# Kernel tuning notes

Hardware: AMD Instinct MI355X
Metric: run time of the kernel (lower is better)

The kernel has to match this reference:

```python
import jax, jax.numpy as jnp
import numpy as np

R = 3
D = 2 * R + 1            # 7 displacements per axis
B, C, H, W = 2, 128, 48, 96
EPS = 1e-5


def conv2d(x, w, stride=1, padding=1):
    return jax.lax.conv_general_dilated(
        x, w, (stride, stride), [(padding, padding), (padding, padding)],
        dimension_numbers=('NCHW', 'OIHW', 'NCHW'))


def deconv2d(x, w, stride=2, padding=1):
    # w: torch ConvTranspose2d layout (I, O, kh, kw)
    wf = jnp.flip(w, (2, 3)).transpose(1, 0, 2, 3)  # -> OIHW, spatially flipped
    p = w.shape[2] - 1 - padding
    return jax.lax.conv_general_dilated(
        x, wf, (1, 1), [(p, p), (p, p)], lhs_dilation=(stride, stride),
        dimension_numbers=('NCHW', 'OIHW', 'NCHW'))


def bn_relu(x, g, b):
    # BatchNorm2d, training-mode statistics (biased variance), then ReLU
    mu = x.mean(axis=(0, 2, 3), keepdims=True)
    var = x.var(axis=(0, 2, 3), keepdims=True)
    xn = (x - mu) * jax.lax.rsqrt(var + EPS)
    return jax.nn.relu(xn * g[None, :, None, None] + b[None, :, None, None])


def grid_sample_zeros(img, gx, gy):
    # img: (B,C,H,W); gx, gy: (B,S) pixel coords. Bilinear, zero padding,
    # align_corners=True (coords already in pixel space -> identity unnormalize).
    b, c, h, w = img.shape
    x0 = jnp.floor(gx)
    y0 = jnp.floor(gy)
    wx = gx - x0
    wy = gy - y0
    imgf = img.reshape(b, c, h * w)

    def corner(xi, yi, wgt):
        valid = (xi >= 0) & (xi < w) & (yi >= 0) & (yi < h)
        xi_c = jnp.clip(xi, 0, w - 1).astype(jnp.int32)
        yi_c = jnp.clip(yi, 0, h - 1).astype(jnp.int32)
        lin = (yi_c * w + xi_c)[:, None, :]            # (B,1,S)
        v = jnp.take_along_axis(imgf, lin, axis=2)     # (B,C,S)
        return v * (wgt * valid)[:, None, :]

    return (corner(x0, y0, (1 - wx) * (1 - wy))
            + corner(x0 + 1, y0, wx * (1 - wy))
            + corner(x0, y0 + 1, (1 - wx) * wy)
            + corner(x0 + 1, y0 + 1, wx * wy))


def setup_inputs() -> dict:
    key = jax.random.key(0)
    ks = jax.random.split(key, 24)
    s = 0.05
    f1 = jax.random.normal(ks[0], (B, C, H, W), dtype=jnp.float32)
    f2 = jax.random.normal(ks[1], (B, C, H, W), dtype=jnp.float32)
    cx = jax.random.uniform(ks[2], (B, 1, H, W), dtype=jnp.float32) * (W - 1)
    cy = jax.random.uniform(ks[3], (B, 1, H, W), dtype=jnp.float32) * (H - 1)
    coords = jnp.concatenate([cx, cy], axis=1)  # (B,2,H,W): [x, y]
    p = {
        'w1': jax.random.normal(ks[4], (96, 2 * C, 3, 3)) * s,
        'g1': jnp.ones((96,)), 'b1': jnp.zeros((96,)),
        'w2': jax.random.normal(ks[5], (128, 96, 3, 3)) * s,
        'g2': jnp.ones((128,)), 'b2': jnp.zeros((128,)),
        'w3': jax.random.normal(ks[6], (128, 128, 3, 3)) * s,
        'g3': jnp.ones((128,)), 'b3': jnp.zeros((128,)),
        'w4': jax.random.normal(ks[7], (64, 128, 3, 3)) * s,
        'g4': jnp.ones((64,)), 'b4': jnp.zeros((64,)),
        'w5': jax.random.normal(ks[8], (64, 32, 4, 4)) * s,  # ConvTranspose (I,O,kh,kw)
        'g5': jnp.ones((32,)), 'b5': jnp.zeros((32,)),
        'w6': jax.random.normal(ks[9], (1, 32, 3, 3)) * s,
        'b6': jnp.zeros((1,)),
        'dap_w': jnp.eye(D * D, dtype=jnp.float32),  # identity init
    }
    return {'f1': f1, 'f2': f2, 'coords': coords, **p}


def reference(f1, f2, coords, w1, g1, b1, w2, g2, b2, w3, g3, b3,
              w4, g4, b4, w5, g5, b5, w6, b6, dap_w):
    b, c, h, w = f1.shape
    dx = jnp.linspace(-R, R, D)
    delta = jnp.stack(jnp.meshgrid(dx, dx, indexing='ij'), axis=-1)  # (D,D,2)
    cen = (coords.transpose(0, 2, 3, 1).reshape(b, 1, h, 1, w, 2)
           + delta.reshape(1, D, 1, D, 1, 2))                        # (B,D,H,D,W,2)
    gx = cen[..., 0].reshape(b, -1)
    gy = cen[..., 1].reshape(b, -1)
    f2s = grid_sample_zeros(f2, gx, gy).reshape(b, c, D, h, D, w)
    f2s = f2s.transpose(0, 2, 4, 1, 3, 5)                            # (B,D,D,C,H,W)
    f1e = jnp.broadcast_to(f1[:, None, None], (b, D, D, c, h, w))
    corr = jnp.concatenate([f1e, f2s], axis=3).reshape(b * D * D, 2 * c, h, w)
    x = bn_relu(conv2d(corr, w1), g1, b1)
    x = bn_relu(conv2d(x, w2, stride=2), g2, b2)
    x = bn_relu(conv2d(x, w3), g3, b3)
    x = bn_relu(conv2d(x, w4), g4, b4)
    x = bn_relu(deconv2d(x, w5), g5, b5)
    x = conv2d(x, w6) + b6[None, :, None, None]
    cost = x.reshape(b, D * D, h, w)
    cost = jnp.einsum('ed,bdhw->behw', dap_w, cost)  # DAP 1x1 conv, no bias
    return cost  # (B, (2r+1)^2, H, W)
```

## Files before the change

kernel.cpp:

```cpp
#include <hip/hip_runtime.h>
#include <hip/hip_bf16.h>

using bf16 = __hip_bfloat16;
typedef __attribute__((ext_vector_type(8))) short s8v;
typedef __attribute__((ext_vector_type(4))) float f4v;
typedef __attribute__((ext_vector_type(16))) float f16v;

static constexpr int Bb = 2, Hh = 48, Ww = 96;
static constexpr int HW = Hh * Ww;
static constexpr int DD = 49, Nn = Bb * DD;
static constexpr int H2 = 24, W2 = 48, HW2 = H2 * W2;

static constexpr size_t off_wf1a = 0;
static constexpr size_t off_wf1b = 221184;
static constexpr size_t off_wf3  = 442368;
static constexpr size_t off_wf2  = 737280;
static constexpr size_t off_wf4  = 958464;
static constexpr size_t off_wf5  = 1105920;
static constexpr size_t off_f1t  = 1171456;
static constexpr size_t off_y1a  = 3530752;
static constexpr size_t off_stats= 7069696;
static constexpr size_t off_f2s  = 7079936;
static constexpr size_t off_y1   = 122685440;
static constexpr size_t off_f2t  = off_y1;
static constexpr size_t off_y2   = off_f2s;
static constexpr size_t off_y3   = off_f2s + 28901376;
static constexpr size_t off_y4   = off_f2s + 57802752;
static constexpr size_t off_y5   = off_f2s + 72253440;
static constexpr size_t off_y6   = off_f2s + 101154816;
static constexpr size_t WS_NEEDED = 209389568;

__device__ __forceinline__ float bf2f(unsigned short h) {
  return __uint_as_float(((unsigned)h) << 16);
}
__device__ __forceinline__ unsigned short f2bf(float f) {
  __hip_bfloat16 h = __float2bfloat16(f);
  union { __hip_bfloat16 x; unsigned short u; } cv; cv.x = h; return cv.u;
}
template<bool EN>
__device__ __forceinline__ uint4 bn8(uint4 v, const float* a, const float* b, int c0) {
  if constexpr (!EN) return v;
  union { uint4 u; unsigned short h[8]; } X; X.u = v;
#pragma unroll
  for (int i = 0; i < 8; ++i) {
    float f = fmaxf(bf2f(X.h[i]) * a[c0 + i] + b[c0 + i], 0.f);
    X.h[i] = f2bf(f);
  }
  return X.u;
}
__device__ __forceinline__ s8v as_s8v(uint4 v) {
  union { uint4 u; s8v s; } cv; cv.u = v; return cv.s;
}
__device__ __forceinline__ int swz(int icl) { return ((icl >> 1) ^ (icl >> 3)) & 3; }

__global__ __launch_bounds__(256) void zero_k(float* __restrict__ p, int n) {
  int i = blockIdx.x * 256 + threadIdx.x;
  if (i < n) p[i] = 0.f;
}

__global__ __launch_bounds__(256) void tr_f2_k(const float* __restrict__ f2, float* __restrict__ f2t) {
  int o = blockIdx.x * 256 + threadIdx.x;
  if (o >= 2 * HW * 16) return;
  int c8 = o & 15; int pos = (o >> 4) % HW; int b = o / (HW * 16);
  float v[8];
#pragma unroll
  for (int i = 0; i < 8; ++i) v[i] = f2[((size_t)(b * 128 + c8 * 8 + i)) * HW + pos];
  float* dst = f2t + ((size_t)b * HW + pos) * 128 + c8 * 8;
#pragma unroll
  for (int i = 0; i < 8; ++i) dst[i] = v[i];
}

__global__ __launch_bounds__(256) void tr_f1_k(const float* __restrict__ f1, bf16* __restrict__ f1t) {
  int o = blockIdx.x * 256 + threadIdx.x;
  if (o >= 2 * HW * 16) return;
  int c8 = o & 15; int pos = (o >> 4) % HW; int b = o / (HW * 16);
  union { uint4 u; unsigned short h[8]; } Y;
#pragma unroll
  for (int i = 0; i < 8; ++i) Y.h[i] = f2bf(f1[((size_t)(b * 128 + c8 * 8 + i)) * HW + pos]);
  *(uint4*)(f1t + ((size_t)b * HW + pos) * 128 + c8 * 8) = Y.u;
}

__global__ __launch_bounds__(256)
void prep32_k(const float* __restrict__ w, uint4* __restrict__ wf, int NT, int CINT, int ciOff) {
  int idx = blockIdx.x * 256 + threadIdx.x;
  int total = 9 * 2 * 4 * NT * 64;
  if (idx >= total) return;
  int ocl = idx & 31; int lh = (idx >> 5) & 1;
  int q = idx >> 6; int nt = q % NT; int rest = q / NT;
  int ks = rest & 3; int cih = (rest >> 2) & 1; int khw = rest >> 3;
  int oc = nt * 32 + ocl;
  union { uint4 u; unsigned short h[8]; } Y;
#pragma unroll
  for (int i = 0; i < 8; ++i) {
    int ci = ciOff + cih * 64 + ks * 16 + lh * 8 + i;
    Y.h[i] = f2bf(w[((size_t)oc * CINT + ci) * 9 + khw]);
  }
  wf[idx] = Y.u;
}

__global__ __launch_bounds__(256)
void prep16_k(const float* __restrict__ w, uint4* __restrict__ wf, int NT, int CINT,
              int NSTAGE, int CPS, int KPS) {
  int idx = blockIdx.x * 256 + threadIdx.x;
  int total = 9 * NSTAGE * KPS * NT * 64;
  if (idx >= total) return;
  int ocl = idx & 15; int lg = (idx >> 4) & 3;
  int q = idx >> 6; int nt = q % NT; int q2 = q / NT;
  int ks = q2 % KPS; int q3 = q2 / KPS;
  int st = q3 % NSTAGE; int khw = q3 / NSTAGE;
  int oc = nt * 16 + ocl;
  union { uint4 u; unsigned short h[8]; } Y;
#pragma unroll
  for (int i = 0; i < 8; ++i) {
    int ci = st * CPS + ks * 32 + lg * 8 + i;
    Y.h[i] = f2bf(w[((size_t)oc * CINT + ci) * 9 + khw]);
  }
  wf[idx] = Y.u;
}

__global__ __launch_bounds__(256)
void prep_w5_k(const float* __restrict__ w5, uint4* __restrict__ wf) {
  int idx = blockIdx.x * 256 + threadIdx.x;
  if (idx >= 4096) return;
  int ocl = idx & 15; int lg = (idx >> 4) & 3;
  int nt = (idx >> 6) & 1; int ks = (idx >> 7) & 7; int p = idx >> 10;
  int ph = p >> 1, pw = p & 1;
  int t = ks >> 2, u = (ks >> 1) & 1;
  int kh = 3 - ph - 2 * t, kw = 3 - pw - 2 * u;
  int oc = nt * 16 + ocl;
  union { uint4 u4; unsigned short h[8]; } Y;
#pragma unroll
  for (int i = 0; i < 8; ++i) {
    int ci = (ks & 1) * 32 + lg * 8 + i;
    Y.h[i] = f2bf(w5[(((size_t)ci * 32 + oc) * 4 + kh) * 4 + kw]);
  }
  wf[idx] = Y.u4;
}

__global__ __launch_bounds__(256)
void sample_k(const float* __restrict__ f2t, const float* __restrict__ coords,
              bf16* __restrict__ f2s) {
  int wv = blockIdx.x * 4 + (threadIdx.x >> 6);
  int lane = threadIdx.x & 63;
  int p0 = wv * 32;
  for (int k = 0; k < 32; ++k) {
    int P = p0 + k;
    int hw = P % HW; int n = P / HW;
    int b = n / DD, d = n % DD;
    float gx = coords[(size_t)b * 2 * HW + hw] + (float)(d / 7 - 3);
    float gy = coords[((size_t)b * 2 + 1) * HW + hw] + (float)(d % 7 - 3);
    float x0f = floorf(gx), y0f = floorf(gy);
    float wx = gx - x0f, wy = gy - y0f;
    int x0 = (int)x0f, y0 = (int)y0f;
    const float* base = f2t + (size_t)b * HW * 128;
    float r0 = 0.f, r1 = 0.f;
#pragma unroll
    for (int c = 0; c < 4; ++c) {
      int xi = x0 + (c & 1), yi = y0 + (c >> 1);
      float wgt = ((c & 1) ? wx : 1.f - wx) * ((c >> 1) ? wy : 1.f - wy);
      if (xi < 0 || xi >= Ww || yi < 0 || yi >= Hh) wgt = 0.f;
      int xc = min(max(xi, 0), Ww - 1), yc = min(max(yi, 0), Hh - 1);
      const float* pv = base + ((size_t)(yc * Ww + xc)) * 128 + 2 * lane;
      r0 += wgt * pv[0];
      r1 += wgt * pv[1];
    }
    unsigned pack = (unsigned)f2bf(r0) | ((unsigned)f2bf(r1) << 16);
    ((unsigned*)f2s)[(size_t)P * 64 + lane] = pack;
  }
}

template<int NLD, int NTHR, int NGRAN, int IC, int CIN>
__device__ __forceinline__ void stage_issue(const bf16* __restrict__ in, size_t inbase,
    int ih0, int iw0, int HI, int WI, int ksl, int tid, uint4 (&stg)[NLD]) {
#pragma unroll
  for (int t = 0; t < NLD; ++t) {
    int idx = tid + t * NTHR;
    uint4 v = make_uint4(0u, 0u, 0u, 0u);
    if (idx < NGRAN) {
      int h8 = idx & 3; int pix = idx >> 2;
      int icl = pix % IC, ihl = pix / IC;
      int ih = ih0 + ihl, iw = iw0 + icl;
      if (ih >= 0 && ih < HI && iw >= 0 && iw < WI)
        v = *(const uint4*)(in + inbase + ((size_t)(ih * WI + iw)) * CIN + ksl * 32 + h8 * 8);
    }
    stg[t] = v;
  }
}

template<int NLD, int NTHR, int NGRAN, int IC, int ROWB, bool HAS_BN>
__device__ __forceinline__ void stage_commit(char* __restrict__ lds,
    const float* __restrict__ a, const float* __restrict__ b,
    int ih0, int iw0, int HI, int WI, int ksl, int tid, uint4 (&stg)[NLD]) {
#pragma unroll
  for (int t = 0; t < NLD; ++t) {
    int idx = tid + t * NTHR;
    if (idx < NGRAN) {
      int h8 = idx & 3; int pix = idx >> 2;
      int icl = pix % IC, ihl = pix / IC;
      uint4 v = stg[t];
      if constexpr (HAS_BN) {
        int ih = ih0 + ihl, iw = iw0 + icl;
        if (ih >= 0 && ih < HI && iw >= 0 && iw < WI) v = bn8<true>(v, a, b, ksl * 32 + h8 * 8);
      }
      int g = h8 ^ swz(icl);
      *(uint4*)(lds + (ihl * IC + icl) * ROWB + g * 16) = v;
    }
  }
}

template<int COUT, int NT, int MT, int NB, int GR, int GC, int CIN,
         bool OUTF32, bool HAS_BASE, bool HAS_BN, bool HAS_STATS>
__global__ __launch_bounds__(((GR * GC) / MT) * (NT / NB) * 64)
void conv32_k(const bf16* __restrict__ in, const uint4* __restrict__ wf,
              void* __restrict__ outv, const float* __restrict__ base,
              const float* __restrict__ bn_a, const float* __restrict__ bn_b,
              float* __restrict__ stats, int N, int H, int W, int DIV) {
  constexpr int NW = ((GR * GC) / MT) * (NT / NB);
  constexpr int NTHR = NW * 64;
  constexpr int BR = GR * 2, BC = GC * 16;
  constexpr int IR = BR + 2, IC = BC + 2;
  constexpr int NSL = CIN / 32;
  constexpr int NGRAN = IR * IC * 4;
  constexpr int NLD = (NGRAN + NTHR - 1) / NTHR;
  __shared__ __align__(16) char lds[IR * IC * 64];

  const int tid = threadIdx.x;
  const int lane = tid & 63;
  const int wv = tid >> 6;
  const int lm = lane & 31, lh = lane >> 5;
  const int dh = lm >> 4, dw = lm & 15;
  constexpr int NG = NT / NB;
  const int mg = wv / NG, ng = wv % NG;

  const int tW = W / BC, tH = H / BR;
  const int tile = blockIdx.x % (tH * tW);
  const int n = blockIdx.x / (tH * tW);
  const int oh0 = (tile / tW) * BR, ow0 = (tile % tW) * BC;
  const int ih0 = oh0 - 1, iw0 = ow0 - 1;
  const size_t inbase = (size_t)n * H * W * CIN;

  int trA[MT], tcA[MT];
#pragma unroll
  for (int i = 0; i < MT; ++i) { int mt = mg * MT + i; trA[i] = mt / GC; tcA[i] = mt % GC; }

  f16v acc[MT][NB];
#pragma unroll
  for (int i = 0; i < MT; ++i)
#pragma unroll
    for (int j = 0; j < NB; ++j)
#pragma unroll
      for (int r = 0; r < 16; ++r) acc[i][j][r] = 0.f;

  {
    uint4 stg0[NLD];
    stage_issue<NLD, NTHR, NGRAN, IC, CIN>(in, inbase, ih0, iw0, H, W, 0, tid, stg0);
    stage_commit<NLD, NTHR, NGRAN, IC, 64, HAS_BN>(lds, bn_a, bn_b, ih0, iw0, H, W, 0, tid, stg0);
  }
  __syncthreads();

#pragma unroll
  for (int ksl = 0; ksl < NSL; ++ksl) {
    uint4 stgN[NLD];
    if (ksl + 1 < NSL)
      stage_issue<NLD, NTHR, NGRAN, IC, CIN>(in, inbase, ih0, iw0, H, W, ksl + 1, tid, stgN);

#pragma unroll
    for (int khw = 0; khw < 9; ++khw) {
      const int kh = khw / 3, kw = khw % 3;
      const uint4* wfp = wf + (size_t)(khw * 2 + (ksl >> 1)) * (NT * 256);
#pragma unroll
      for (int ks = 0; ks < 2; ++ks) {
        s8v Af[MT], Bf[NB];
#pragma unroll
        for (int i = 0; i < MT; ++i) {
          int rl = trA[i] * 2 + dh + kh;
          int cl = tcA[i] * 16 + dw + kw;
          int g = (ks * 2 + lh) ^ swz(cl);
          Af[i] = *(const s8v*)(lds + (rl * IC + cl) * 64 + g * 16);
        }
        int ks4 = (ksl & 1) * 2 + ks;
#pragma unroll
        for (int j = 0; j < NB; ++j)
          Bf[j] = as_s8v(wfp[(ks4 * NT + ng * NB + j) * 64 + lane]);
#pragma unroll
        for (int i = 0; i < MT; ++i)
#pragma unroll
          for (int j = 0; j < NB; ++j)
            acc[i][j] = __builtin_amdgcn_mfma_f32_32x32x16_bf16(Af[i], Bf[j], acc[i][j], 0, 0, 0);
      }
    }

    if (ksl + 1 < NSL) {
      __syncthreads();
      stage_commit<NLD, NTHR, NGRAN, IC, 64, HAS_BN>(lds, bn_a, bn_b, ih0, iw0, H, W, ksl + 1, tid, stgN);
      __syncthreads();
    }
  }

  const size_t obase = (size_t)n * H * W * COUT;
  const float* bptr = nullptr;
  if constexpr (HAS_BASE) bptr = base + (size_t)(n / DIV) * H * W * COUT;

  float sacc[NB], qacc[NB];
#pragma unroll
  for (int j = 0; j < NB; ++j) { sacc[j] = 0.f; qacc[j] = 0.f; }

#pragma unroll
  for (int i = 0; i < MT; ++i) {
#pragma unroll
    for (int j = 0; j < NB; ++j) {
      int oc = (ng * NB + j) * 32 + lm;
#pragma unroll
      for (int r = 0; r < 16; ++r) {
        int row = (r & 3) + 8 * (r >> 2) + 4 * lh;
        int oh = oh0 + trA[i] * 2 + (row >> 4);
        int ow = ow0 + tcA[i] * 16 + (row & 15);
        size_t pix = (size_t)(oh * W + ow);
        float v = acc[i][j][r];
        if constexpr (HAS_BASE) v += bptr[pix * COUT + oc];
        if constexpr (HAS_STATS) { sacc[j] += v; qacc[j] += v * v; }
        if constexpr (OUTF32) ((float*)outv)[obase + pix * COUT + oc] = v;
        else ((bf16*)outv)[obase + pix * COUT + oc] = __float2bfloat16(v);
      }
    }
  }

  if constexpr (HAS_STATS) {
    __shared__ float sred[2 * COUT];
    for (int i = tid; i < 2 * COUT; i += NTHR) sred[i] = 0.f;
    __syncthreads();
#pragma unroll
    for (int j = 0; j < NB; ++j) {
      int oc = (ng * NB + j) * 32 + lm;
      atomicAdd(&sred[oc], sacc[j]);
      atomicAdd(&sred[COUT + oc], qacc[j]);
    }
    __syncthreads();
    for (int i = tid; i < 2 * COUT; i += NTHR) atomicAdd(&stats[i], sred[i]);
  }
}

template<int COUT, int NT, int MT, int NB, int GR, int GC, int STRIDE,
         int CINT, bool HAS_BN, bool HAS_STATS>
__global__ __launch_bounds__(((GR * GC) / MT) * (NT / NB) * 64)
void conv16_k(const bf16* __restrict__ in, const uint4* __restrict__ wf,
              bf16* __restrict__ out, const float* __restrict__ bn_a,
              const float* __restrict__ bn_b, float* __restrict__ stats,
              int N, int HO, int WO, int HI, int WI) {
  constexpr int NW = ((GR * GC) / MT) * (NT / NB);
  constexpr int NTHR = NW * 64;
  constexpr int BR = GR, BC = GC * 16;
  constexpr int IR = STRIDE * (BR - 1) + 3;
  constexpr int IC = STRIDE * (BC - 1) + 3 + (STRIDE == 2 ? 1 : 0);
  constexpr int ROWB = (STRIDE == 2) ? 80 : 64;
  constexpr int NSL = CINT / 32;
  constexpr int NGRAN = IR * IC * 4;
  constexpr int NLD = (NGRAN + NTHR - 1) / NTHR;
  __shared__ __align__(16) char lds[IR * IC * ROWB];

  const int tid = threadIdx.x;
  const int lane = tid & 63;
  const int wv = tid >> 6;
  const int lm = lane & 15, lg = lane >> 4;
  constexpr int NG = NT / NB;
  const int mg = wv / NG, ng = wv % NG;

  const int tW = WO / BC, tH = HO / BR;
  const int tile = blockIdx.x % (tH * tW);
  const int n = blockIdx.x / (tH * tW);
  const int oh0 = (tile / tW) * BR, ow0 = (tile % tW) * BC;
  const int ih0 = STRIDE * oh0 - 1, iw0 = STRIDE * ow0 - 1;
  const size_t inbase = (size_t)n * HI * WI * CINT;

  int trA[MT], tcA[MT];
#pragma unroll
  for (int i = 0; i < MT; ++i) { int mt = mg * MT + i; trA[i] = mt / GC; tcA[i] = mt % GC; }

  f4v acc[MT][NB];
#pragma unroll
  for (int i = 0; i < MT; ++i)
#pragma unroll
    for (int j = 0; j < NB; ++j)
#pragma unroll
      for (int r = 0; r < 4; ++r) acc[i][j][r] = 0.f;

  {
    uint4 stg0[NLD];
    stage_issue<NLD, NTHR, NGRAN, IC, CINT>(in, inbase, ih0, iw0, HI, WI, 0, tid, stg0);
    stage_commit<NLD, NTHR, NGRAN, IC, ROWB, HAS_BN>(lds, bn_a, bn_b, ih0, iw0, HI, WI, 0, tid, stg0);
  }
  __syncthreads();

#pragma unroll
  for (int ksl = 0; ksl < NSL; ++ksl) {
    uint4 stgN[NLD];
    if (ksl + 1 < NSL)
      stage_issue<NLD, NTHR, NGRAN, IC, CINT>(in, inbase, ih0, iw0, HI, WI, ksl + 1, tid, stgN);

#pragma unroll
    for (int khw = 0; khw < 9; ++khw) {
      const int kh = khw / 3, kw = khw % 3;
      const uint4* wfp = wf + (size_t)(khw * NSL + ksl) * (NT * 64);
      s8v Af[MT], Bf[NB];
#pragma unroll
      for (int i = 0; i < MT; ++i) {
        int rl = STRIDE * trA[i] + kh;
        int cl = STRIDE * (tcA[i] * 16 + lm) + kw;
        int g = lg ^ swz(cl);
        Af[i] = *(const s8v*)(lds + (rl * IC + cl) * ROWB + g * 16);
      }
#pragma unroll
      for (int j = 0; j < NB; ++j)
        Bf[j] = as_s8v(wfp[(ng * NB + j) * 64 + lane]);
#pragma unroll
      for (int i = 0; i < MT; ++i)
#pragma unroll
        for (int j = 0; j < NB; ++j)
          acc[i][j] = __builtin_amdgcn_mfma_f32_16x16x32_bf16(Af[i], Bf[j], acc[i][j], 0, 0, 0);
    }

    if (ksl + 1 < NSL) {
      __syncthreads();
      stage_commit<NLD, NTHR, NGRAN, IC, ROWB, HAS_BN>(lds, bn_a, bn_b, ih0, iw0, HI, WI, ksl + 1, tid, stgN);
      __syncthreads();
    }
  }

  const size_t obase = (size_t)n * HO * WO * COUT;
  float sacc[NB], qacc[NB];
#pragma unroll
  for (int j = 0; j < NB; ++j) { sacc[j] = 0.f; qacc[j] = 0.f; }

#pragma unroll
  for (int i = 0; i < MT; ++i) {
#pragma unroll
    for (int j = 0; j < NB; ++j) {
      int oc = (ng * NB + j) * 16 + lm;
#pragma unroll
      for (int r = 0; r < 4; ++r) {
        int oh = oh0 + trA[i];
        int ow = ow0 + tcA[i] * 16 + lg * 4 + r;
        float v = acc[i][j][r];
        if constexpr (HAS_STATS) { sacc[j] += v; qacc[j] += v * v; }
        out[obase + (size_t)(oh * WO + ow) * COUT + oc] = __float2bfloat16(v);
      }
    }
  }

  if constexpr (HAS_STATS) {
    __shared__ float sred[2 * COUT];
    for (int i = tid; i < 2 * COUT; i += NTHR) sred[i] = 0.f;
    __syncthreads();
#pragma unroll
    for (int j = 0; j < NB; ++j) {
      int oc = (ng * NB + j) * 16 + lm;
      atomicAdd(&sred[oc], sacc[j]);
      atomicAdd(&sred[COUT + oc], qacc[j]);
    }
    __syncthreads();
    for (int i = tid; i < 2 * COUT; i += NTHR) atomicAdd(&stats[i], sred[i]);
  }
}

__global__ __launch_bounds__(256)
void deconv16_k(const bf16* __restrict__ in, const uint4* __restrict__ wf5,
                bf16* __restrict__ out, const float* __restrict__ a4,
                const float* __restrict__ b4, float* __restrict__ stats) {
  constexpr int IR = 6, IC = 50, INB = IR * IC * 128;
  __shared__ __align__(16) char lds[INB];
  __shared__ float sred[64];
  const int tid = threadIdx.x;
  const int lane = tid & 63, wv = tid >> 6;
  const int lm = lane & 15, lg = lane >> 4;
  const int n = blockIdx.x / 6;
  const int qh0 = (blockIdx.x % 6) * 4;
  const size_t ibase = (size_t)n * HW2 * 64;

  for (int idx = tid; idx < 64; idx += 256) sred[idx] = 0.f;

  for (int idx = tid; idx < IR * IC * 8; idx += 256) {
    int h8 = idx & 7; int icl = (idx >> 3) % IC; int ihl = (idx >> 3) / IC;
    int ih = qh0 - 1 + ihl, iw = -1 + icl;
    uint4 v = make_uint4(0u, 0u, 0u, 0u);
    if (ih >= 0 && ih < H2 && iw >= 0 && iw < W2) {
      v = *(const uint4*)(in + ibase + ((size_t)(ih * W2 + iw)) * 64 + h8 * 8);
      v = bn8<true>(v, a4, b4, h8 * 8);
    }
    int bbyte = (ihl * IC + icl) * 128 + h8 * 16;
    bbyte ^= (icl & 7) << 4;
    *(uint4*)(lds + bbyte) = v;
  }
  __syncthreads();

  int trA[3], tcA[3];
#pragma unroll
  for (int i = 0; i < 3; ++i) { int mt = wv * 3 + i; trA[i] = mt / 3; tcA[i] = mt % 3; }

  float sacc[2], qacc[2];
  sacc[0] = sacc[1] = qacc[0] = qacc[1] = 0.f;

  for (int p = 0; p < 4; ++p) {
    const int ph = p >> 1, pw = p & 1;
    f4v acc[3][2];
#pragma unroll
    for (int i = 0; i < 3; ++i)
#pragma unroll
      for (int j = 0; j < 2; ++j)
#pragma unroll
        for (int r = 0; r < 4; ++r) acc[i][j][r] = 0.f;
#pragma unroll
    for (int ks = 0; ks < 8; ++ks) {
      int t = ks >> 2, u = (ks >> 1) & 1, cb = ks & 1;
      s8v Af[3], Bf[2];
#pragma unroll
      for (int i = 0; i < 3; ++i) {
        int rl = trA[i] + t + ph;
        int cl = tcA[i] * 16 + lm + u + pw;
        int bbyte = (rl * IC + cl) * 128 + cb * 64 + lg * 16;
        bbyte ^= (cl & 7) << 4;
        Af[i] = *(const s8v*)(lds + bbyte);
      }
#pragma unroll
      for (int j = 0; j < 2; ++j)
        Bf[j] = as_s8v(wf5[p * 1024 + (ks * 2 + j) * 64 + lg * 16 + lm]);
#pragma unroll
      for (int i = 0; i < 3; ++i)
#pragma unroll
        for (int j = 0; j < 2; ++j)
          acc[i][j] = __builtin_amdgcn_mfma_f32_16x16x32_bf16(Af[i], Bf[j], acc[i][j], 0, 0, 0);
    }
#pragma unroll
    for (int i = 0; i < 3; ++i) {
#pragma unroll
      for (int j = 0; j < 2; ++j) {
        int oc = j * 16 + lm;
#pragma unroll
        for (int r = 0; r < 4; ++r) {
          int qh = qh0 + trA[i];
          int qw = tcA[i] * 16 + lg * 4 + r;
          int oh = 2 * qh + ph, ow = 2 * qw + pw;
          float v = acc[i][j][r];
          sacc[j] += v; qacc[j] += v * v;
          out[((size_t)n * HW + oh * Ww + ow) * 32 + oc] = __float2bfloat16(v);
        }
      }
    }
  }

  __syncthreads();
#pragma unroll
  for (int j = 0; j < 2; ++j) {
    int oc = j * 16 + lm;
    atomicAdd(&sred[oc], sacc[j]);
    atomicAdd(&sred[32 + oc], qacc[j]);
  }
  __syncthreads();
  for (int i = tid; i < 64; i += 256) atomicAdd(&stats[i], sred[i]);
}

__global__ void bnfin_k(const float* __restrict__ sums, const float* __restrict__ gamma,
                        const float* __restrict__ beta, float* __restrict__ ab, int C, float invCnt) {
  int c = blockIdx.x * blockDim.x + threadIdx.x;
  if (c >= C) return;
  float mean = sums[c] * invCnt;
  float var = sums[C + c] * invCnt - mean * mean;
  float a = gamma[c] * rsqrtf(var + 1e-5f);
  ab[c] = a;
  ab[C + c] = beta[c] - mean * a;
}

__global__ __launch_bounds__(256)
void conv6_k(const bf16* __restrict__ y5, const float* __restrict__ w6,
             const float* __restrict__ b6, const float* __restrict__ a5,
             const float* __restrict__ bb5, float* __restrict__ y6) {
  int o = blockIdx.x * 256 + threadIdx.x;
  if (o >= Nn * HW) return;
  int hw = o % HW; int n = o / HW;
  int h = hw / Ww, w = hw % Ww;
  float acc = b6[0];
  for (int kh = 0; kh < 3; ++kh) {
    int ih = h - 1 + kh; if (ih < 0 || ih >= Hh) continue;
    for (int kw = 0; kw < 3; ++kw) {
      int iw = w - 1 + kw; if (iw < 0 || iw >= Ww) continue;
      const bf16* p = y5 + ((size_t)n * HW + ih * Ww + iw) * 32;
      int khw = kh * 3 + kw;
#pragma unroll
      for (int c8 = 0; c8 < 4; ++c8) {
        union { uint4 u; unsigned short hh[8]; } X;
        X.u = *(const uint4*)(p + c8 * 8);
#pragma unroll
        for (int i = 0; i < 8; ++i) {
          int c = c8 * 8 + i;
          float f = fmaxf(bf2f(X.hh[i]) * a5[c] + bb5[c], 0.f);
          acc += f * w6[c * 9 + khw];
        }
      }
    }
  }
  y6[o] = acc;
}

__global__ __launch_bounds__(256)
void dap_k(const float* __restrict__ y6, const float* __restrict__ dap, float* __restrict__ out) {
  int o = blockIdx.x * 256 + threadIdx.x;
  if (o >= Bb * DD * HW) return;
  int hw = o % HW;
  int e = (o / HW) % DD;
  int b = o / (HW * DD);
  float s = 0.f;
#pragma unroll 7
  for (int d = 0; d < DD; ++d) s += dap[e * DD + d] * y6[((size_t)(b * DD + d)) * HW + hw];
  out[o] = s;
}

extern "C" void kernel_launch(void* const* d_in, const int* in_sizes, int n_in,
                              void* d_out, int out_size, void* d_ws, size_t ws_size,
                              hipStream_t stream) {
  const float* f1 = (const float*)d_in[0];
  const float* f2 = (const float*)d_in[1];
  const float* coords = (const float*)d_in[2];
  const float* w1 = (const float*)d_in[3];
  const float* g1 = (const float*)d_in[4];
  const float* b1 = (const float*)d_in[5];
  const float* w2 = (const float*)d_in[6];
  const float* g2 = (const float*)d_in[7];
  const float* b2 = (const float*)d_in[8];
  const float* w3 = (const float*)d_in[9];
  const float* g3 = (const float*)d_in[10];
  const float* b3 = (const float*)d_in[11];
  const float* w4 = (const float*)d_in[12];
  const float* g4 = (const float*)d_in[13];
  const float* b4 = (const float*)d_in[14];
  const float* w5 = (const float*)d_in[15];
  const float* g5 = (const float*)d_in[16];
  const float* b5 = (const float*)d_in[17];
  const float* w6 = (const float*)d_in[18];
  const float* b6 = (const float*)d_in[19];
  const float* dap = (const float*)d_in[20];
  float* out = (float*)d_out;
  char* ws = (char*)d_ws;
  if (ws_size < WS_NEEDED) return;

  uint4* wf1a = (uint4*)(ws + off_wf1a);
  uint4* wf1b = (uint4*)(ws + off_wf1b);
  uint4* wf3 = (uint4*)(ws + off_wf3);
  uint4* wf2 = (uint4*)(ws + off_wf2);
  uint4* wf4 = (uint4*)(ws + off_wf4);
  uint4* wf5 = (uint4*)(ws + off_wf5);
  bf16* f1t = (bf16*)(ws + off_f1t);
  float* y1a = (float*)(ws + off_y1a);
  float* f2t = (float*)(ws + off_f2t);
  bf16* f2s = (bf16*)(ws + off_f2s);
  bf16* y1 = (bf16*)(ws + off_y1);
  bf16* y2 = (bf16*)(ws + off_y2);
  bf16* y3 = (bf16*)(ws + off_y3);
  bf16* y4 = (bf16*)(ws + off_y4);
  bf16* y5 = (bf16*)(ws + off_y5);
  float* y6 = (float*)(ws + off_y6);
  float* st0 = (float*)(ws + off_stats) + 0 * 512;
  float* st1 = (float*)(ws + off_stats) + 1 * 512;
  float* st2 = (float*)(ws + off_stats) + 2 * 512;
  float* st3 = (float*)(ws + off_stats) + 3 * 512;
  float* st4 = (float*)(ws + off_stats) + 4 * 512;

  zero_k<<<10, 256, 0, stream>>>((float*)(ws + off_stats), 2560);

  tr_f2_k<<<576, 256, 0, stream>>>(f2, f2t);
  tr_f1_k<<<576, 256, 0, stream>>>(f1, f1t);
  prep32_k<<<54, 256, 0, stream>>>(w1, wf1a, 3, 256, 0);
  prep32_k<<<54, 256, 0, stream>>>(w1, wf1b, 3, 256, 128);
  prep32_k<<<72, 256, 0, stream>>>(w3, wf3, 4, 128, 0);
  prep16_k<<<54, 256, 0, stream>>>(w2, wf2, 8, 96, 3, 32, 1);
  prep16_k<<<36, 256, 0, stream>>>(w4, wf4, 4, 128, 4, 32, 1);
  prep_w5_k<<<16, 256, 0, stream>>>(w5, wf5);

  sample_k<<<3528, 256, 0, stream>>>(f2t, coords, f2s);

  conv32_k<96, 3, 2, 3, 4, 2, 128, true, false, false, false><<<36, 256, 0, stream>>>(
      f1t, wf1a, y1a, nullptr, nullptr, nullptr, nullptr, 2, Hh, Ww, 1);
  conv32_k<96, 3, 2, 3, 4, 2, 128, false, true, false, true><<<1764, 256, 0, stream>>>(
      f2s, wf1b, y1, y1a, nullptr, nullptr, st0, Nn, Hh, Ww, DD);
  bnfin_k<<<1, 256, 0, stream>>>(st0, g1, b1, st0 + 256, 96, 1.f / (98.f * 4608.f));

  conv16_k<128, 8, 3, 4, 2, 3, 2, 96, true, true><<<1176, 256, 0, stream>>>(
      y1, wf2, y2, st0 + 256, st0 + 256 + 96, st1, Nn, H2, W2, Hh, Ww);
  bnfin_k<<<1, 256, 0, stream>>>(st1, g2, b2, st1 + 256, 128, 1.f / (98.f * 1152.f));

  conv32_k<128, 4, 3, 2, 2, 3, 128, false, false, true, true><<<588, 256, 0, stream>>>(
      y2, wf3, y3, nullptr, st1 + 256, st1 + 256 + 128, st2, Nn, H2, W2, 1);
  bnfin_k<<<1, 256, 0, stream>>>(st2, g3, b3, st2 + 256, 128, 1.f / (98.f * 1152.f));

  conv16_k<64, 4, 3, 4, 4, 3, 1, 128, true, true><<<588, 256, 0, stream>>>(
      y3, wf4, y4, st2 + 256, st2 + 256 + 128, st3, Nn, H2, W2, H2, W2);
  bnfin_k<<<1, 256, 0, stream>>>(st3, g4, b4, st3 + 256, 64, 1.f / (98.f * 1152.f));

  deconv16_k<<<588, 256, 0, stream>>>(y4, wf5, y5, st3 + 256, st3 + 256 + 64, st4);
  bnfin_k<<<1, 256, 0, stream>>>(st4, g5, b5, st4 + 256, 32, 1.f / (98.f * 4608.f));

  conv6_k<<<1764, 256, 0, stream>>>(y5, w6, b6, st4 + 256, st4 + 256 + 32, y6);

  dap_k<<<1764, 256, 0, stream>>>(y6, dap, out);
}
```

Before: 686.5 us.

## Pad conv1 inputs, use direct global-to-LDS loads, split sampling per batch, tile conv6/dap

Stores f1 and the sampled f2 in zero-bordered padded NHWC buffers. A new conv1 kernel then streams them into double-buffered LDS with global_load_lds and needs no bounds checks. f2 is transposed to bf16 instead of fp32, which halves the gather traffic in sample_k. Sampling and conv1 now run in two per-batch halves to shrink the f2s workspace and keep it cache-friendlier. conv6 and dap are rewritten to stage their inputs (with BN applied once) and weights in shared memory, which adds extra launches and border-zeroing work.

```diff
diff --git a/kernel.cpp b/kernel.cpp
--- a/kernel.cpp
+++ b/kernel.cpp
@@ -18,17 +18,18 @@
 static constexpr size_t off_wf4  = 958464;
 static constexpr size_t off_wf5  = 1105920;
 static constexpr size_t off_f1t  = 1171456;
-static constexpr size_t off_y1a  = 3530752;
-static constexpr size_t off_stats= 7069696;
-static constexpr size_t off_f2s  = 7079936;
-static constexpr size_t off_y1   = 122685440;
-static constexpr size_t off_f2t  = off_y1;
-static constexpr size_t off_y2   = off_f2s;
-static constexpr size_t off_y3   = off_f2s + 28901376;
-static constexpr size_t off_y4   = off_f2s + 57802752;
-static constexpr size_t off_y5   = off_f2s + 72253440;
-static constexpr size_t off_y6   = off_f2s + 101154816;
-static constexpr size_t WS_NEEDED = 209389568;
+static constexpr size_t off_y1a  = 3680256;
+static constexpr size_t off_stats= 7219200;
+static constexpr size_t off_big  = 7229440;
+static constexpr size_t off_f2s  = off_big;
+static constexpr size_t off_f2tb = off_big + 61465600;
+static constexpr size_t off_y2   = off_big;
+static constexpr size_t off_y3   = off_big + 28901376;
+static constexpr size_t off_y4   = off_big + 57802752;
+static constexpr size_t off_y5   = off_big + 72253440;
+static constexpr size_t off_y6   = off_big + 101154816;
+static constexpr size_t off_y1   = 110190592;
+static constexpr size_t WS_NEEDED = 196894720;
 
 __device__ __forceinline__ float bf2f(unsigned short h) {
   return __uint_as_float(((unsigned)h) << 16);
@@ -52,32 +53,47 @@
   union { uint4 u; s8v s; } cv; cv.u = v; return cv.s;
 }
 __device__ __forceinline__ int swz(int icl) { return ((icl >> 1) ^ (icl >> 3)) & 3; }
+__device__ __forceinline__ int swz6(int cell) { return (cell ^ (cell >> 2)) & 3; }
 
 __global__ __launch_bounds__(256) void zero_k(float* __restrict__ p, int n) {
   int i = blockIdx.x * 256 + threadIdx.x;
   if (i < n) p[i] = 0.f;
 }
 
-__global__ __launch_bounds__(256) void tr_f2_k(const float* __restrict__ f2, float* __restrict__ f2t) {
+__global__ __launch_bounds__(256) void border0_k(bf16* __restrict__ f2s) {
+  int idx = blockIdx.x * 256 + threadIdx.x;
+  if (idx >= 49 * 292) return;
+  int c2 = idx % 292, n = idx / 292;
+  int r, c;
+  if (c2 < 98) { r = 0; c = c2; }
+  else if (c2 < 196) { r = 49; c = c2 - 98; }
+  else if (c2 < 244) { r = c2 - 196 + 1; c = 0; }
+  else { r = c2 - 244 + 1; c = 97; }
+  uint4* p = (uint4*)(f2s + ((size_t)(n * 50 + r) * 98 + c) * 128);
+  uint4 z = make_uint4(0u, 0u, 0u, 0u);
+#pragma unroll
+  for (int i = 0; i < 16; ++i) p[i] = z;
+}
+
+__global__ __launch_bounds__(256) void tr_f2b_k(const float* __restrict__ f2, bf16* __restrict__ f2tb) {
   int o = blockIdx.x * 256 + threadIdx.x;
   if (o >= 2 * HW * 16) return;
   int c8 = o & 15; int pos = (o >> 4) % HW; int b = o / (HW * 16);
-  float v[8];
-#pragma unroll
-  for (int i = 0; i < 8; ++i) v[i] = f2[((size_t)(b * 128 + c8 * 8 + i)) * HW + pos];
-  float* dst = f2t + ((size_t)b * HW + pos) * 128 + c8 * 8;
-#pragma unroll
-  for (int i = 0; i < 8; ++i) dst[i] = v[i];
+  union { uint4 u; unsigned short h[8]; } Y;
+#pragma unroll
+  for (int i = 0; i < 8; ++i) Y.h[i] = f2bf(f2[((size_t)(b * 128 + c8 * 8 + i)) * HW + pos]);
+  *(uint4*)(f2tb + ((size_t)b * HW + pos) * 128 + c8 * 8) = Y.u;
 }
 
 __global__ __launch_bounds__(256) void tr_f1_k(const float* __restrict__ f1, bf16* __restrict__ f1t) {
   int o = blockIdx.x * 256 + threadIdx.x;
   if (o >= 2 * HW * 16) return;
   int c8 = o & 15; int pos = (o >> 4) % HW; int b = o / (HW * 16);
-  union { uint4 u; unsigned short h[8]; } Y;
-#pragma unroll
-  for (int i = 0; i < 8; ++i) Y.h[i] = f2bf(f1[((size_t)(b * 128 + c8 * 8 + i)) * HW + pos]);
-  *(uint4*)(f1t + ((size_t)b * HW + pos) * 128 + c8 * 8) = Y.u;
+  int h = pos / Ww, w = pos % Ww;
+  union { uint4 u; unsigned short h8[8]; } Y;
+#pragma unroll
+  for (int i = 0; i < 8; ++i) Y.h8[i] = f2bf(f1[((size_t)(b * 128 + c8 * 8 + i)) * HW + pos]);
+  *(uint4*)(f1t + ((size_t)(b * 50 + h + 1) * 98 + (w + 1)) * 128 + c8 * 8) = Y.u;
 }
 
 __global__ __launch_bounds__(256)
@@ -138,21 +154,21 @@
 }
 
 __global__ __launch_bounds__(256)
-void sample_k(const float* __restrict__ f2t, const float* __restrict__ coords,
-              bf16* __restrict__ f2s) {
+void sample_k(const bf16* __restrict__ f2tb, const float* __restrict__ coords,
+              bf16* __restrict__ f2s, int half) {
   int wv = blockIdx.x * 4 + (threadIdx.x >> 6);
   int lane = threadIdx.x & 63;
   int p0 = wv * 32;
+  const unsigned* src = (const unsigned*)f2tb + (size_t)half * HW * 64;
+  unsigned* dst = (unsigned*)f2s;
   for (int k = 0; k < 32; ++k) {
     int P = p0 + k;
-    int hw = P % HW; int n = P / HW;
-    int b = n / DD, d = n % DD;
-    float gx = coords[(size_t)b * 2 * HW + hw] + (float)(d / 7 - 3);
-    float gy = coords[((size_t)b * 2 + 1) * HW + hw] + (float)(d % 7 - 3);
+    int hw = P % HW; int nl = P / HW;
+    float gx = coords[(size_t)half * 2 * HW + hw] + (float)(nl / 7 - 3);
+    float gy = coords[((size_t)half * 2 + 1) * HW + hw] + (float)(nl % 7 - 3);
     float x0f = floorf(gx), y0f = floorf(gy);
     float wx = gx - x0f, wy = gy - y0f;
     int x0 = (int)x0f, y0 = (int)y0f;
-    const float* base = f2t + (size_t)b * HW * 128;
     float r0 = 0.f, r1 = 0.f;
 #pragma unroll
     for (int c = 0; c < 4; ++c) {
@@ -160,12 +176,154 @@
       float wgt = ((c & 1) ? wx : 1.f - wx) * ((c >> 1) ? wy : 1.f - wy);
       if (xi < 0 || xi >= Ww || yi < 0 || yi >= Hh) wgt = 0.f;
       int xc = min(max(xi, 0), Ww - 1), yc = min(max(yi, 0), Hh - 1);
-      const float* pv = base + ((size_t)(yc * Ww + xc)) * 128 + 2 * lane;
-      r0 += wgt * pv[0];
-      r1 += wgt * pv[1];
-    }
+      unsigned pv = src[(size_t)(yc * Ww + xc) * 64 + lane];
+      r0 += wgt * bf2f((unsigned short)(pv & 0xffff));
+      r1 += wgt * bf2f((unsigned short)(pv >> 16));
+    }
+    int h = hw / Ww, w = hw % Ww;
     unsigned pack = (unsigned)f2bf(r0) | ((unsigned)f2bf(r1) << 16);
-    ((unsigned*)f2s)[(size_t)P * 64 + lane] = pack;
+    dst[((size_t)(nl * 50 + h + 1) * 98 + (w + 1)) * 64 + lane] = pack;
+  }
+}
+
+template<int COUT, int NT, int MT, int NB, int GR, int GC, bool OUTF32, bool HAS_BASE, bool HAS_STATS>
+__global__ __launch_bounds__(((GR * GC) / MT) * (NT / NB) * 64, 3)
+void conv32gll_k(const bf16* __restrict__ in, const uint4* __restrict__ wf,
+                 void* __restrict__ outv, const float* __restrict__ base,
+                 float* __restrict__ stats, int N, int H, int W) {
+  constexpr int NW = ((GR * GC) / MT) * (NT / NB);
+  constexpr int BR = GR * 2, BC = GC * 16;
+  constexpr int IR = BR + 2, IC = BC + 2;
+  constexpr int NGRAN = IR * IC * 4;
+  constexpr int NCH = (NGRAN + 63) / 64;
+  constexpr int BUFB = NCH * 1024;
+  constexpr int NCHW = (NCH + NW - 1) / NW;
+  __shared__ __align__(16) char lds[2 * BUFB];
+
+  const int tid = threadIdx.x;
+  const int lane = tid & 63;
+  const int wv = tid >> 6;
+  const int lm = lane & 31, lh = lane >> 5;
+  const int dh = lm >> 4, dw = lm & 15;
+  constexpr int NG = NT / NB;
+  const int mg = wv / NG, ng = wv % NG;
+
+  const int tW = W / BC, tH = H / BR;
+  const int tile = blockIdx.x % (tH * tW);
+  const int n = blockIdx.x / (tH * tW);
+  const int oh0 = (tile / tW) * BR, ow0 = (tile % tW) * BC;
+  const int PW = W + 2, PH = H + 2;
+
+  int pixoff[NCHW];
+#pragma unroll
+  for (int k = 0; k < NCHW; ++k) {
+    int c = wv + k * NW;
+    int gi = c * 64 + lane;
+    int cell = gi >> 2; if (cell >= IR * IC) cell = IR * IC - 1;
+    int slot = gi & 3;
+    int row = cell / IC, col = cell % IC;
+    pixoff[k] = ((n * PH + oh0 + row) * PW + ow0 + col) * 128 + (slot ^ swz(col)) * 8;
+  }
+
+  int trA[MT], tcA[MT];
+#pragma unroll
+  for (int i = 0; i < MT; ++i) { int mt = mg * MT + i; trA[i] = mt / GC; tcA[i] = mt % GC; }
+
+  f16v acc[MT][NB];
+#pragma unroll
+  for (int i = 0; i < MT; ++i)
+#pragma unroll
+    for (int j = 0; j < NB; ++j)
+#pragma unroll
+      for (int r = 0; r < 16; ++r) acc[i][j][r] = 0.f;
+
+#pragma unroll
+  for (int k = 0; k < NCHW; ++k) {
+    int c = wv + k * NW;
+    if (c < NCH)
+      __builtin_amdgcn_global_load_lds((const void*)(in + (size_t)pixoff[k]),
+                                       (void*)(lds + c * 1024), 16, 0, 0);
+  }
+  __syncthreads();
+
+#pragma unroll
+  for (int ksl = 0; ksl < 4; ++ksl) {
+    if (ksl < 3) {
+#pragma unroll
+      for (int k = 0; k < NCHW; ++k) {
+        int c = wv + k * NW;
+        if (c < NCH)
+          __builtin_amdgcn_global_load_lds(
+              (const void*)(in + (size_t)pixoff[k] + (ksl + 1) * 32),
+              (void*)(lds + ((ksl + 1) & 1) * BUFB + c * 1024), 16, 0, 0);
+      }
+    }
+    const char* bufp = lds + (ksl & 1) * BUFB;
+#pragma unroll
+    for (int khw = 0; khw < 9; ++khw) {
+      const int kh = khw / 3, kw = khw % 3;
+      const uint4* wfp = wf + (size_t)(khw * 2 + (ksl >> 1)) * (NT * 256);
+#pragma unroll
+      for (int ks = 0; ks < 2; ++ks) {
+        s8v Af[MT], Bf[NB];
+#pragma unroll
+        for (int i = 0; i < MT; ++i) {
+          int rl = trA[i] * 2 + dh + kh;
+          int cl = tcA[i] * 16 + dw + kw;
+          int g = (ks * 2 + lh) ^ swz(cl);
+          Af[i] = *(const s8v*)(bufp + (rl * IC + cl) * 64 + g * 16);
+        }
+        int ks4 = (ksl & 1) * 2 + ks;
+#pragma unroll
+        for (int j = 0; j < NB; ++j)
+          Bf[j] = as_s8v(wfp[(ks4 * NT + ng * NB + j) * 64 + lane]);
+#pragma unroll
+        for (int i = 0; i < MT; ++i)
+#pragma unroll
+          for (int j = 0; j < NB; ++j)
+            acc[i][j] = __builtin_amdgcn_mfma_f32_32x32x16_bf16(Af[i], Bf[j], acc[i][j], 0, 0, 0);
+      }
+    }
+    __syncthreads();
+  }
+
+  const size_t obase = (size_t)n * H * W * COUT;
+  float sacc[NB], qacc[NB];
+#pragma unroll
+  for (int j = 0; j < NB; ++j) { sacc[j] = 0.f; qacc[j] = 0.f; }
+
+#pragma unroll
+  for (int i = 0; i < MT; ++i) {
+#pragma unroll
+    for (int j = 0; j < NB; ++j) {
+      int oc = (ng * NB + j) * 32 + lm;
+#pragma unroll
+      for (int r = 0; r < 16; ++r) {
+        int row = (r & 3) + 8 * (r >> 2) + 4 * lh;
+        int oh = oh0 + trA[i] * 2 + (row >> 4);
+        int ow = ow0 + tcA[i] * 16 + (row & 15);
+        size_t pix = (size_t)(oh * W + ow);
+        float v = acc[i][j][r];
+        if constexpr (HAS_BASE) v += base[pix * COUT + oc];
+        if constexpr (HAS_STATS) { sacc[j] += v; qacc[j] += v * v; }
+        if constexpr (OUTF32) ((float*)outv)[obase + pix * COUT + oc] = v;
+        else ((bf16*)outv)[obase + pix * COUT + oc] = __float2bfloat16(v);
+      }
+    }
+  }
+
+  if constexpr (HAS_STATS) {
+    __shared__ float sred[2 * COUT];
+    for (int i = tid; i < 2 * COUT; i += NW * 64) sred[i] = 0.f;
+    __syncthreads();
+#pragma unroll
+    for (int j = 0; j < NB; ++j) {
+      int oc = (ng * NB + j) * 32 + lm;
+      atomicAdd(&sred[oc], sacc[j]);
+      atomicAdd(&sred[COUT + oc], qacc[j]);
+    }
+    __syncthreads();
+    for (int i = tid; i < 2 * COUT; i += NW * 64) atomicAdd(&stats[i], sred[i]);
   }
 }
 
@@ -209,12 +367,12 @@
 }
 
 template<int COUT, int NT, int MT, int NB, int GR, int GC, int CIN,
-         bool OUTF32, bool HAS_BASE, bool HAS_BN, bool HAS_STATS>
+         bool OUTF32, bool HAS_BN, bool HAS_STATS>
 __global__ __launch_bounds__(((GR * GC) / MT) * (NT / NB) * 64)
 void conv32_k(const bf16* __restrict__ in, const uint4* __restrict__ wf,
-              void* __restrict__ outv, const float* __restrict__ base,
+              void* __restrict__ outv,
               const float* __restrict__ bn_a, const float* __restrict__ bn_b,
-              float* __restrict__ stats, int N, int H, int W, int DIV) {
+              float* __restrict__ stats, int N, int H, int W) {
   constexpr int NW = ((GR * GC) / MT) * (NT / NB);
   constexpr int NTHR = NW * 64;
   constexpr int BR = GR * 2, BC = GC * 16;
@@ -298,9 +456,6 @@
   }
 
   const size_t obase = (size_t)n * H * W * COUT;
-  const float* bptr = nullptr;
-  if constexpr (HAS_BASE) bptr = base + (size_t)(n / DIV) * H * W * COUT;
-
   float sacc[NB], qacc[NB];
 #pragma unroll
   for (int j = 0; j < NB; ++j) { sacc[j] = 0.f; qacc[j] = 0.f; }
@@ -317,7 +472,6 @@
         int ow = ow0 + tcA[i] * 16 + (row & 15);
         size_t pix = (size_t)(oh * W + ow);
         float v = acc[i][j][r];
-        if constexpr (HAS_BASE) v += bptr[pix * COUT + oc];
         if constexpr (HAS_STATS) { sacc[j] += v; qacc[j] += v * v; }
         if constexpr (OUTF32) ((float*)outv)[obase + pix * COUT + oc] = v;
         else ((bf16*)outv)[obase + pix * COUT + oc] = __float2bfloat16(v);
@@ -569,48 +723,66 @@
   ab[C + c] = beta[c] - mean * a;
 }
 
-__global__ __launch_bounds__(256)
+__global__ __launch_bounds__(384)
 void conv6_k(const bf16* __restrict__ y5, const float* __restrict__ w6,
              const float* __restrict__ b6, const float* __restrict__ a5,
              const float* __restrict__ bb5, float* __restrict__ y6) {
-  int o = blockIdx.x * 256 + threadIdx.x;
-  if (o >= Nn * HW) return;
-  int hw = o % HW; int n = o / HW;
-  int h = hw / Ww, w = hw % Ww;
+  __shared__ __align__(16) char l6[6 * 98 * 64];
+  __shared__ float w6s[288];
+  const int tid = threadIdx.x;
+  const int n = blockIdx.x / 12, qh0 = (blockIdx.x % 12) * 4;
+  if (tid < 288) w6s[tid] = w6[tid];
+  for (int idx = tid; idx < 6 * 98 * 4; idx += 384) {
+    int g = idx & 3, cell = idx >> 2;
+    int icl = cell % 98, ihl = cell / 98;
+    int ih = qh0 - 1 + ihl, iw = icl - 1;
+    uint4 v = make_uint4(0u, 0u, 0u, 0u);
+    if (ih >= 0 && ih < Hh && iw >= 0 && iw < Ww) {
+      v = *(const uint4*)(y5 + ((size_t)n * HW + ih * Ww + iw) * 32 + g * 8);
+      v = bn8<true>(v, a5, bb5, g * 8);
+    }
+    *(uint4*)(l6 + cell * 64 + (g ^ swz6(cell)) * 16) = v;
+  }
+  __syncthreads();
+
+  const int trow = tid / 96, ow = tid % 96;
   float acc = b6[0];
+#pragma unroll
   for (int kh = 0; kh < 3; ++kh) {
-    int ih = h - 1 + kh; if (ih < 0 || ih >= Hh) continue;
+#pragma unroll
     for (int kw = 0; kw < 3; ++kw) {
-      int iw = w - 1 + kw; if (iw < 0 || iw >= Ww) continue;
-      const bf16* p = y5 + ((size_t)n * HW + ih * Ww + iw) * 32;
+      int cell = (trow + kh) * 98 + ow + kw;
       int khw = kh * 3 + kw;
 #pragma unroll
       for (int c8 = 0; c8 < 4; ++c8) {
-        union { uint4 u; unsigned short hh[8]; } X;
-        X.u = *(const uint4*)(p + c8 * 8);
-#pragma unroll
-        for (int i = 0; i < 8; ++i) {
-          int c = c8 * 8 + i;
-          float f = fmaxf(bf2f(X.hh[i]) * a5[c] + bb5[c], 0.f);
-          acc += f * w6[c * 9 + khw];
-        }
-      }
-    }
-  }
-  y6[o] = acc;
+        union { uint4 u; unsigned short h[8]; } X;
+        X.u = *(const uint4*)(l6 + cell * 64 + (c8 ^ swz6(cell)) * 16);
+#pragma unroll
+        for (int i = 0; i < 8; ++i)
+          acc += bf2f(X.h[i]) * w6s[(c8 * 8 + i) * 9 + khw];
+      }
+    }
+  }
+  y6[(size_t)n * HW + (qh0 + trow) * Ww + ow] = acc;
 }
 
 __global__ __launch_bounds__(256)
 void dap_k(const float* __restrict__ y6, const float* __restrict__ dap, float* __restrict__ out) {
-  int o = blockIdx.x * 256 + threadIdx.x;
-  if (o >= Bb * DD * HW) return;
-  int hw = o % HW;
-  int e = (o / HW) % DD;
-  int b = o / (HW * DD);
-  float s = 0.f;
+  __shared__ float sh[49 * 64];
+  const int tid = threadIdx.x;
+  const int b = blockIdx.x / 72, t0 = (blockIdx.x % 72) * 64;
+  for (int idx = tid; idx < 49 * 64; idx += 256) {
+    int d = idx >> 6, x = idx & 63;
+    sh[idx] = y6[((size_t)(b * 49 + d)) * HW + t0 + x];
+  }
+  __syncthreads();
+  for (int oidx = tid; oidx < 49 * 64; oidx += 256) {
+    int e = oidx >> 6, x = oidx & 63;
+    float s = 0.f;
 #pragma unroll 7
-  for (int d = 0; d < DD; ++d) s += dap[e * DD + d] * y6[((size_t)(b * DD + d)) * HW + hw];
-  out[o] = s;
+    for (int d = 0; d < 49; ++d) s += dap[e * 49 + d] * sh[(d << 6) + x];
+    out[((size_t)(b * 49 + e)) * HW + t0 + x] = s;
+  }
 }
 
 extern "C" void kernel_launch(void* const* d_in, const int* in_sizes, int n_in,
@@ -649,7 +821,7 @@
   uint4* wf5 = (uint4*)(ws + off_wf5);
   bf16* f1t = (bf16*)(ws + off_f1t);
   float* y1a = (float*)(ws + off_y1a);
-  float* f2t = (float*)(ws + off_f2t);
+  bf16* f2tb = (bf16*)(ws + off_f2tb);
   bf16* f2s = (bf16*)(ws + off_f2s);
   bf16* y1 = (bf16*)(ws + off_y1);
   bf16* y2 = (bf16*)(ws + off_y2);
@@ -664,8 +836,9 @@
   float* st4 = (float*)(ws + off_stats) + 4 * 512;
 
   zero_k<<<10, 256, 0, stream>>>((float*)(ws + off_stats), 2560);
-
-  tr_f2_k<<<576, 256, 0, stream>>>(f2, f2t);
+  zero_k<<<2451, 256, 0, stream>>>((float*)f1t, 627200);
+
+  tr_f2b_k<<<576, 256, 0, stream>>>(f2, f2tb);
   tr_f1_k<<<576, 256, 0, stream>>>(f1, f1t);
   prep32_k<<<54, 256, 0, stream>>>(w1, wf1a, 3, 256, 0);
   prep32_k<<<54, 256, 0, stream>>>(w1, wf1b, 3, 256, 128);
@@ -674,20 +847,25 @@
   prep16_k<<<36, 256, 0, stream>>>(w4, wf4, 4, 128, 4, 32, 1);
   prep_w5_k<<<16, 256, 0, stream>>>(w5, wf5);
 
-  sample_k<<<3528, 256, 0, stream>>>(f2t, coords, f2s);
-
-  conv32_k<96, 3, 2, 3, 4, 2, 128, true, false, false, false><<<36, 256, 0, stream>>>(
-      f1t, wf1a, y1a, nullptr, nullptr, nullptr, nullptr, 2, Hh, Ww, 1);
-  conv32_k<96, 3, 2, 3, 4, 2, 128, false, true, false, true><<<1764, 256, 0, stream>>>(
-      f2s, wf1b, y1, y1a, nullptr, nullptr, st0, Nn, Hh, Ww, DD);
+  border0_k<<<56, 256, 0, stream>>>(f2s);
+
+  conv32gll_k<96, 3, 2, 3, 4, 2, true, false, false><<<36, 256, 0, stream>>>(
+      f1t, wf1a, y1a, nullptr, nullptr, 2, Hh, Ww);
+
+  for (int half = 0; half < 2; ++half) {
+    sample_k<<<1764, 256, 0, stream>>>(f2tb, coords, f2s, half);
+    conv32gll_k<96, 3, 2, 3, 4, 2, false, true, true><<<882, 256, 0, stream>>>(
+        f2s, wf1b, y1 + (size_t)half * 49 * HW * 96, y1a + (size_t)half * HW * 96,
+        st0, 49, Hh, Ww);
+  }
   bnfin_k<<<1, 256, 0, stream>>>(st0, g1, b1, st0 + 256, 96, 1.f / (98.f * 4608.f));
 
   conv16_k<128, 8, 3, 4, 2, 3, 2, 96, true, true><<<1176, 256, 0, stream>>>(
       y1, wf2, y2, st0 + 256, st0 + 256 + 96, st1, Nn, H2, W2, Hh, Ww);
   bnfin_k<<<1, 256, 0, stream>>>(st1, g2, b2, st1 + 256, 128, 1.f / (98.f * 1152.f));
 
-  conv32_k<128, 4, 3, 2, 2, 3, 128, false, false, true, true><<<588, 256, 0, stream>>>(
-      y2, wf3, y3, nullptr, st1 + 256, st1 + 256 + 128, st2, Nn, H2, W2, 1);
+  conv32_k<128, 4, 3, 2, 2, 3, 128, false, true, true><<<588, 256, 0, stream>>>(
+      y2, wf3, y3, st1 + 256, st1 + 256 + 128, st2, Nn, H2, W2);
   bnfin_k<<<1, 256, 0, stream>>>(st2, g3, b3, st2 + 256, 128, 1.f / (98.f * 1152.f));
 
   conv16_k<64, 4, 3, 4, 4, 3, 1, 128, true, true><<<588, 256, 0, stream>>>(
@@ -697,7 +875,7 @@
   deconv16_k<<<588, 256, 0, stream>>>(y4, wf5, y5, st3 + 256, st3 + 256 + 64, st4);
   bnfin_k<<<1, 256, 0, stream>>>(st4, g5, b5, st4 + 256, 32, 1.f / (98.f * 4608.f));
 
-  conv6_k<<<1764, 256, 0, stream>>>(y5, w6, b6, st4 + 256, st4 + 256 + 32, y6);
-
-  dap_k<<<1764, 256, 0, stream>>>(y6, dap, out);
-}
+  conv6_k<<<1176, 384, 0, stream>>>(y5, w6, b6, st4 + 256, st4 + 256 + 32, y6);
+
+  dap_k<<<144, 256, 0, stream>>>(y6, dap, out);
+}
```

After: 841.9 us. 22.6% more time.
